# Performance work log

Measured on AMD Instinct MI355X. Metric: run time of the kernel, lower is better.

## Reference

```python
import jax, jax.numpy as jnp
import numpy as np
import math

B, T, XD, H, DD, P = 512, 256, 128, 512, 16, 32
IN = 2 * XD + DD  # GRUCell input size


def _init(key, shape, fan):
    stdv = 1.0 / math.sqrt(fan)
    return jax.random.uniform(key, shape, jnp.float32, -stdv, stdv)


def setup_inputs() -> dict:
    key = jax.random.key(0)
    ks = jax.random.split(key, 32)
    inp = {
        "values": jax.random.normal(ks[0], (B, T, XD), jnp.float32),
        "lens": jnp.full((B,), T, dtype=jnp.int32),  # lens[0] == max_len
        "static": jax.random.normal(ks[1], (B, DD), jnp.float32),
        "times": jax.random.uniform(ks[2], (B, T, XD), jnp.float32),
        "masks": (jax.random.uniform(ks[3], (B, T, XD)) < 0.8).astype(jnp.float32),
        "prototype": jax.random.normal(ks[4], (P, H), jnp.float32),
        "proto": True,
        # temp_decay_h: Linear(x_dim -> hidden), custom uniform(-1/sqrt(H), 1/sqrt(H))
        "Wd": _init(ks[5], (H, XD), H), "bd": _init(ks[6], (H,), XD),
        # hist_reg: Linear(hidden -> x_dim)
        "Wh": _init(ks[7], (XD, H), H), "bh": _init(ks[8], (XD,), H),
        "Wf": _init(ks[9], (XD, XD), XD), "bf": _init(ks[10], (XD,), XD),
        # ProtoAttn Q/K/V: Linear(hidden -> hidden)
        "Wq": _init(ks[11], (H, H), H), "bq": _init(ks[12], (H,), H),
        "Wk": _init(ks[13], (H, H), H), "bk": _init(ks[14], (H,), H),
        "Wv": _init(ks[15], (H, H), H), "bv": _init(ks[16], (H,), H),
        # gating W: Linear(2*hidden -> 1)
        "Wg": _init(ks[17], (1, 2 * H), 2 * H), "bg": _init(ks[18], (1,), 2 * H),
        # GRUCell
        "Wih": _init(ks[19], (3 * H, IN), H), "Whh": _init(ks[20], (3 * H, H), H),
        "bih": _init(ks[21], (3 * H,), H), "bhh": _init(ks[22], (3 * H,), H),
    }
    return inp


def _forward(values, static, times, masks, prototype,
             Wd, bd, Wh, bh, Wf, bf, Wq, bq, Wk, bk, Wv, bv, Wg, bg,
             Wih, Whh, bih, bhh, lens, proto):
    feat_m = 1.0 - jnp.eye(XD, dtype=values.dtype)  # zero-diagonal mask
    gamma = jnp.exp(-jax.nn.relu(jnp.einsum("btx,hx->bth", times, Wd) + bd))
    # attention key/value do not depend on h -> precompute
    keyp = prototype @ Wk.T + bk      # [P,H]
    valp = prototype @ Wv.T + bv      # [P,H]
    scale = 1.0 / math.sqrt(P)
    valid = (jnp.arange(T)[:, None] < lens[None, :]).astype(values.dtype)  # [T,B]

    xs = (jnp.swapaxes(values, 0, 1),  # [T,B,XD]
          jnp.swapaxes(masks, 0, 1),   # [T,B,XD]
          jnp.swapaxes(gamma, 0, 1),   # [T,B,H]
          valid[:, :, None])           # [T,B,1]

    h0 = jnp.zeros((B, H), values.dtype)
    xh0 = jnp.zeros((B, XD), values.dtype)

    def step(carry, xt):
        h, x_h = carry
        x, m, g, v = xt
        if proto:
            q = h @ Wq.T + bq                          # [B,H]
            score = (q @ keyp.T) * scale               # [B,P]
            attn = jax.nn.softmax(score, axis=-1)      # dropout omitted (eval)
            h1 = attn @ valp                           # [B,H]
            alpha = jax.nn.sigmoid(jnp.concatenate([h, h1], axis=1) @ Wg.T + bg)
            h = alpha * h + (1.0 - alpha) * h1
        h = h * g
        x_h = jnp.where(v > 0, h @ Wh.T + bh, x_h)
        x_c = m * x + (1.0 - m) * x_h
        z_h = x_c @ (Wf * feat_m).T + bf
        z_c = m * x + (1.0 - m) * z_h
        inp = jnp.concatenate([z_c, m, static], axis=1)
        gx = inp @ Wih.T + bih
        gh = h @ Whh.T + bhh
        xr, xz, xn = jnp.split(gx, 3, axis=1)
        hr, hz, hn = jnp.split(gh, 3, axis=1)
        r = jax.nn.sigmoid(xr + hr)
        z = jax.nn.sigmoid(xz + hz)
        n = jnp.tanh(xn + r * hn)
        h_new = (1.0 - z) * n + z * h
        h = jnp.where(v > 0, h_new, h)
        return (h, x_h), (h, x_c, z_c)

    (hN, _), (hs, x_cs, z_cs) = jax.lax.scan(step, (h0, xh0), xs)
    hs = jnp.swapaxes(hs, 0, 1)
    x_cs = jnp.swapaxes(x_cs, 0, 1)
    z_cs = jnp.swapaxes(z_cs, 0, 1)
    return hs, hN, x_cs, z_cs


def reference(values, lens, static, times, masks, prototype, proto,
              Wd, bd, Wh, bh, Wf, bf, Wq, bq, Wk, bk, Wv, bv, Wg, bg,
              Wih, Whh, bih, bhh):
    return _forward(values, static, times, masks, prototype,
                    Wd, bd, Wh, bh, Wf, bf, Wq, bq, Wk, bk, Wv, bv, Wg, bg,
                    Wih, Whh, bih, bhh, lens, bool(proto))
```

## Files before the change

kernel.cpp:

```cpp
#include <hip/hip_runtime.h>

#define NB 256
#define NT 512

#define Bv 512
#define Tv 256
#define XDv 128
#define Hv 512
#define DDv 16
#define Pv 32

typedef short s8 __attribute__((ext_vector_type(8)));
typedef float f4 __attribute__((ext_vector_type(4)));

#define OFF_KEYP 2048
#define OFF_VALP (OFF_KEYP + 16384)
#define OFF_MF   (OFF_VALP + 16384)
#define OFF_C    (OFF_MF + 16384)
#define OFF_VWG  (OFF_C + 32)
#define OFF_FRG  (OFF_VWG + 32)
#define US_WD   0
#define US_MS   65536
#define US_VP   81920
#define US_WH   98304
#define US_WF   163840
#define US_WHH  180224
#define US_WIH  966656
#define US_END  1409024
#define OFF_H   (OFF_FRG + (US_END/2))

#define OUT_HS  0
#define OUT_HN  (Bv*Tv*Hv)
#define OUT_XCS (OUT_HN + Bv*Hv)
#define OUT_ZCS (OUT_XCS + Bv*Tv*XDv)

struct Smem {
  unsigned short hA[32*520];
  unsigned short tA[32*136];
  unsigned short xcA[32*136];
  unsigned short inpA[32*296];
  unsigned short aA[32*40];
  unsigned short mA[32*136];
  unsigned short xhS[32*128];
  float xvS[32*132];
  float scS[32*34];
  float ghS[3*32*33];
  float gxS[3*32*33];
  float hp32[32*32];
  float al[32], rsm[32], cS[32], vwgS[32];
};

__device__ __forceinline__ unsigned short f2b(float f) {
  union { float f; unsigned int u; } x{f};
  unsigned int r = x.u + 0x7fffu + ((x.u >> 16) & 1u);
  return (unsigned short)(r >> 16);
}
__device__ __forceinline__ float b2f(unsigned short u) {
  union { unsigned int u; float f; } x{(unsigned int)u << 16};
  return x.f;
}
__device__ __forceinline__ float sig_f(float x) { return 1.f / (1.f + __expf(-x)); }
__device__ __forceinline__ float tanh_f(float x) {
  x = fminf(fmaxf(x, -15.f), 15.f);
  float e = __expf(2.f * x);
  return (e - 1.f) / (e + 1.f);
}
__device__ __forceinline__ s8 pack8(const float* p) {
  f4 a = *(const f4*)p; f4 b = *(const f4*)(p + 4);
  s8 r;
  r[0]=(short)f2b(a[0]); r[1]=(short)f2b(a[1]); r[2]=(short)f2b(a[2]); r[3]=(short)f2b(a[3]);
  r[4]=(short)f2b(b[0]); r[5]=(short)f2b(b[1]); r[6]=(short)f2b(b[2]); r[7]=(short)f2b(b[3]);
  return r;
}

__device__ __forceinline__ void gridbar(unsigned int* bar, unsigned int& lgen, int bid) {
  __syncthreads();
  if (threadIdx.x == 0) {
    __threadfence();
    const unsigned int target = ++lgen;
    unsigned int* grp = bar + (bid >> 4)*16;
    const unsigned int a =
        __hip_atomic_fetch_add(grp, 1u, __ATOMIC_ACQ_REL, __HIP_MEMORY_SCOPE_AGENT);
    if (a == 15u) {
      __hip_atomic_store(grp, 0u, __ATOMIC_RELAXED, __HIP_MEMORY_SCOPE_AGENT);
      const unsigned int r =
          __hip_atomic_fetch_add(bar + 384, 1u, __ATOMIC_ACQ_REL, __HIP_MEMORY_SCOPE_AGENT);
      if (r == 15u) {
        __hip_atomic_store(bar + 384, 0u, __ATOMIC_RELAXED, __HIP_MEMORY_SCOPE_AGENT);
        __hip_atomic_store(bar + 400, target, __ATOMIC_RELEASE, __HIP_MEMORY_SCOPE_AGENT);
      }
    }
    while (__hip_atomic_load(bar + 400, __ATOMIC_RELAXED, __HIP_MEMORY_SCOPE_AGENT) < target)
      __builtin_amdgcn_s_sleep(2);
    __threadfence();
  }
  __syncthreads();
}

__device__ __forceinline__ void rgbar_nf(unsigned int* bar, unsigned int& lgen, int rg) {
  __syncthreads();
  if (threadIdx.x == 0) {
    const unsigned int target = ++lgen;
    unsigned int* cnt = bar + 512 + rg*64;
    unsigned int* flg = cnt + 32;
    const unsigned int a =
        __hip_atomic_fetch_add(cnt, 1u, __ATOMIC_RELAXED, __HIP_MEMORY_SCOPE_AGENT);
    if (a == 15u) {
      __hip_atomic_store(cnt, 0u, __ATOMIC_RELAXED, __HIP_MEMORY_SCOPE_AGENT);
      asm volatile("s_waitcnt vmcnt(0)" ::: "memory");
      __hip_atomic_store(flg, target, __ATOMIC_RELAXED, __HIP_MEMORY_SCOPE_AGENT);
    } else {
      while (__hip_atomic_load(flg, __ATOMIC_RELAXED, __HIP_MEMORY_SCOPE_AGENT) < target)
        __builtin_amdgcn_s_sleep(2);
    }
  }
  __syncthreads();
}

#define SWZ(DST, NTILES, KT_, EXPR)                                            \
  { const int tot = (NTILES)*(KT_)*512;                                        \
    for (int f = gtid; f < tot; f += NB*NT) {                                  \
      const int e = f & 7, lane_ = (f >> 3) & 63, rem = f >> 9;                \
      const int kt = rem % (KT_), nt = rem / (KT_);                            \
      const int n = nt*16 + (lane_ & 15);                                      \
      const int k = kt*32 + ((lane_ >> 4) & 3)*8 + e;                          \
      (DST)[f] = f2b((EXPR));                                                  \
    } }

#define MFMA(a,b,c) __builtin_amdgcn_mfma_f32_16x16x32_bf16((a),(b),(c),0,0,0)
#define FRAG(P,idx) (*(const s8*)&(P)[((size_t)(idx))*8])

__global__ __launch_bounds__(NT, 2)
void rits_main(const float* __restrict__ values, const int* __restrict__ lens,
               const float* __restrict__ statc, const float* __restrict__ times,
               const float* __restrict__ masks, const float* __restrict__ prototype,
               const int* __restrict__ protoflag,
               const float* __restrict__ Wd, const float* __restrict__ bd,
               const float* __restrict__ Wh, const float* __restrict__ bh,
               const float* __restrict__ Wf, const float* __restrict__ bf,
               const float* __restrict__ Wq, const float* __restrict__ bq,
               const float* __restrict__ Wk, const float* __restrict__ bk,
               const float* __restrict__ Wv, const float* __restrict__ bv,
               const float* __restrict__ Wg, const float* __restrict__ bg,
               const float* __restrict__ Wih, const float* __restrict__ Whh,
               const float* __restrict__ bih, const float* __restrict__ bhh,
               float* __restrict__ out, float* __restrict__ ws)
{
  const int bid = blockIdx.x, tid = threadIdx.x;
  const int gtid = bid*NT + tid;
  const int wv = tid >> 6, ln = tid & 63;
  const int l15 = ln & 15, l4 = ln >> 4;
  const int cg = (bid & 7)*2 + ((bid >> 7) & 1);
  const int rg = (bid >> 3) & 15;
  const int r0 = rg*32, c0 = cg*32;
  unsigned int* bar = (unsigned int*)ws;
  unsigned int lgenG = 0, lgenR = 0;
  unsigned short* frg = (unsigned short*)(ws + OFF_FRG);
  const unsigned short* wdW  = frg + US_WD;
  const unsigned short* msW  = frg + US_MS;
  const unsigned short* vpW  = frg + US_VP;
  const unsigned short* whW  = frg + US_WH;
  const unsigned short* wfW  = frg + US_WF;
  const unsigned short* whhW = frg + US_WHH;
  const unsigned short* wihW = frg + US_WIH;
  unsigned int* wsH = (unsigned int*)(ws + OFF_H);

  __shared__ Smem L;
  const bool proto = protoflag[0] != 0;
  const float scale = 0.17677669529663687f;

  for (int o = gtid; o < 2*Pv*Hv; o += NB*NT) {
    const int which = o >> 14, rem = o & 16383;
    const int p = rem >> 9, j = rem & 511;
    const float* W = which ? Wv : Wk;
    const float* bb = which ? bv : bk;
    const float* pr = prototype + p*Hv;
    const float* wr = W + j*Hv;
    float s = bb[j];
    #pragma unroll 4
    for (int k = 0; k < Hv; ++k) s += pr[k]*wr[k];
    ws[(which ? OFF_VALP : OFF_KEYP) + p*Hv + j] = s;
  }
  SWZ(frg + US_WD, 32, 4,  Wd[n*XDv + k])
  SWZ(frg + US_WH, 8, 16,  Wh[n*Hv + k])
  SWZ(frg + US_WF, 8, 4,   (n == k ? 0.f : Wf[n*XDv + k]))
  SWZ(frg + US_WHH, 96, 16,
      Whh[((size_t)(n >> 9)*Hv + (((n >> 5) & 15)*32 + ((n >> 4) & 1)*16 + (n & 15)))*Hv + k])
  SWZ(frg + US_WIH, 96, 9,
      (k < 272 ? Wih[((size_t)(n >> 9)*Hv + (((n >> 5) & 15)*32 + ((n >> 4) & 1)*16 + (n & 15)))*272 + k] : 0.f))
  gridbar(bar, lgenG, bid);

  {
    const float* keyp = ws + OFF_KEYP;
    const float* valp = ws + OFF_VALP;
    for (int o = gtid; o < Pv*Hv; o += NB*NT) {
      const int p = o >> 9, kc = o & 511;
      float s = 0.f;
      #pragma unroll 4
      for (int j = 0; j < Hv; ++j) s += keyp[p*Hv + j]*Wq[j*Hv + kc];
      ws[OFF_MF + o] = s;
    }
    if (gtid < 32) {
      float s = 0.f;
      for (int j = 0; j < Hv; ++j) s += bq[j]*keyp[gtid*Hv + j];
      ws[OFF_C + gtid] = s;
    } else if (gtid < 64) {
      const int p = gtid - 32;
      float s = 0.f;
      for (int j = 0; j < Hv; ++j) s += valp[p*Hv + j]*Wg[Hv + j];
      ws[OFF_VWG + p] = s;
    }
  }
  gridbar(bar, lgenG, bid);

  SWZ(frg + US_MS, 2, 16, (ws + OFF_MF)[n*Hv + k])
  SWZ(frg + US_VP, 32, 1, (ws + OFF_VALP)[k*Hv + n])
  gridbar(bar, lgenG, bid);

  for (int o = tid; o < 32*128; o += NT) L.xhS[o] = 0;
  if (tid < 32) { L.cS[tid] = ws[OFF_C + tid]; L.vwgS[tid] = ws[OFF_VWG + tid]; }
  for (int o = tid; o < 32*40; o += NT) {
    const int row = o / 40, cc = o % 40;
    L.inpA[row*296 + 256 + cc] =
        (cc < DDv) ? f2b(statc[(r0 + row)*DDv + cc]) : (unsigned short)0;
  }

  const int xcol = wv*16 + l15;
  const float bhR = bh[xcol], bfR = bf[xcol];
  int lensA[8];
  #pragma unroll
  for (int rt = 0; rt < 2; ++rt)
    #pragma unroll
    for (int i = 0; i < 4; ++i)
      lensA[rt*4 + i] = lens[r0 + rt*16 + l4*4 + i];
  float wgr[8];
  if (wv >= 4) {
    #pragma unroll
    for (int e = 0; e < 8; ++e) wgr[e] = Wg[ln*8 + e];
  }
  f4 bdW;
  #pragma unroll
  for (int q = 0; q < 4; ++q) bdW[q] = bd[wv*64 + q*16 + l15];
  const int crow = tid >> 5, cjj = tid & 31;
  float bihR[3], bhhR[3];
  #pragma unroll
  for (int g = 0; g < 3; ++g) { bihR[g] = bih[g*Hv + c0 + cjj]; bhhR[g] = bhh[g*Hv + c0 + cjj]; }
  const int lensG0 = lens[r0 + crow], lensG1 = lens[r0 + crow + 16];
  const float bg0 = bg[0];

  float pv[8], pm[8], pt[8];
  #pragma unroll
  for (int i = 0; i < 8; ++i) {
    const int o = i*NT + tid, row = o >> 7, col = o & 127;
    const size_t a = ((size_t)(r0 + row)*Tv + 0)*XDv + col;
    pv[i] = values[a]; pm[i] = masks[a]; pt[i] = times[a];
  }
  __syncthreads();

  for (int t = 0; t < Tv; ++t) {
    #pragma unroll
    for (int i = 0; i < 8; ++i) {
      const int o = i*NT + tid, row = o >> 7, col = o & 127;
      L.xvS[row*132 + col] = pv[i];
      L.mA[row*136 + col]  = f2b(pm[i]);
      L.tA[row*136 + col]  = f2b(pt[i]);
    }
    {
      const int tn = (t + 1 < Tv) ? t + 1 : t;
      #pragma unroll
      for (int i = 0; i < 8; ++i) {
        const int o = i*NT + tid, row = o >> 7, col = o & 127;
        const size_t a = ((size_t)(r0 + row)*Tv + tn)*XDv + col;
        pv[i] = values[a]; pm[i] = masks[a]; pt[i] = times[a];
      }
    }
    if (t > 0) {
      const unsigned int* src = wsH + ((t - 1) & 1)*131072;
      #pragma unroll
      for (int i = 0; i < 16; ++i) {
        const int o = i*NT + tid, row = o >> 8, cp = o & 255;
        const unsigned int v = __hip_atomic_load(
            &src[(size_t)(r0 + row)*256 + cp], __ATOMIC_RELAXED, __HIP_MEMORY_SCOPE_AGENT);
        ((unsigned int*)&L.hA[row*520])[cp] = v;
      }
    } else {
      for (int o = tid; o < 32*256; o += NT) {
        const int row = o >> 8, cp = o & 255;
        ((unsigned int*)&L.hA[row*520])[cp] = 0u;
      }
    }
    __syncthreads();

    if (proto) {
      if (wv < 4) {
        const int rt = wv >> 1, nt = wv & 1;
        f4 acc = {0.f,0.f,0.f,0.f};
        #pragma unroll
        for (int kt = 0; kt < 16; ++kt) {
          s8 a = *(const s8*)&L.hA[(rt*16 + l15)*520 + kt*32 + l4*8];
          acc = MFMA(a, FRAG(msW, (nt*16 + kt)*64 + ln), acc);
        }
        #pragma unroll
        for (int i = 0; i < 4; ++i)
          L.scS[(rt*16 + l4*4 + i)*34 + nt*16 + l15] = acc[i];
      } else {
        #pragma unroll
        for (int rr = 0; rr < 8; ++rr) {
          const int row = (wv - 4)*8 + rr;
          s8 hv8 = *(const s8*)&L.hA[row*520 + ln*8];
          float s = 0.f;
          #pragma unroll
          for (int e = 0; e < 8; ++e) s += b2f((unsigned short)hv8[e]) * wgr[e];
          s += __shfl_xor(s, 1);  s += __shfl_xor(s, 2);  s += __shfl_xor(s, 4);
          s += __shfl_xor(s, 8);  s += __shfl_xor(s, 16); s += __shfl_xor(s, 32);
          if (ln == 0) L.scS[row*34 + 32] = s;
        }
      }
    }
    __syncthreads();

    if (proto && wv == 0 && ln < 32) {
      const int r = ln;
      float mx = -1e30f;
      #pragma unroll 8
      for (int p = 0; p < 32; ++p)
        mx = fmaxf(mx, (L.scS[r*34 + p] + L.cS[p]) * scale);
      float sm = 0.f, a1 = 0.f;
      #pragma unroll 8
      for (int p = 0; p < 32; ++p) {
        float e = __expf((L.scS[r*34 + p] + L.cS[p]) * scale - mx);
        sm += e; a1 += e * L.vwgS[p];
        L.aA[r*40 + p] = f2b(e);
      }
      const float rs = 1.f / sm;
      L.rsm[r] = rs;
      L.al[r] = sig_f(L.scS[r*34 + 32] + a1*rs + bg0);
    }
    __syncthreads();

    #pragma unroll
    for (int q = 0; q < 4; ++q) {
      const int nt = wv*4 + q;
      const int col = nt*16 + l15;
      #pragma unroll
      for (int rt = 0; rt < 2; ++rt) {
        f4 g = {0.f,0.f,0.f,0.f};
        #pragma unroll
        for (int kt = 0; kt < 4; ++kt) {
          s8 a = *(const s8*)&L.tA[(rt*16 + l15)*136 + kt*32 + l4*8];
          g = MFMA(a, FRAG(wdW, (nt*4 + kt)*64 + ln), g);
        }
        f4 h1 = {0.f,0.f,0.f,0.f};
        if (proto) {
          s8 a = *(const s8*)&L.aA[(rt*16 + l15)*40 + l4*8];
          h1 = MFMA(a, FRAG(vpW, nt*64 + ln), h1);
        }
        #pragma unroll
        for (int i = 0; i < 4; ++i) {
          const int row = rt*16 + l4*4 + i;
          const float gam = __expf(-fmaxf(g[i] + bdW[q], 0.f));
          const float hbf = b2f(L.hA[row*520 + col]);
          float hp;
          if (proto) {
            const float av = L.al[row];
            hp = (av*hbf + (1.f - av)*h1[i]*L.rsm[row]) * gam;
          } else hp = hbf * gam;
          L.hA[row*520 + col] = f2b(hp);
          const unsigned cc = (unsigned)(col - c0);
          if (cc < 32u) L.hp32[row*32 + cc] = hp;
        }
      }
    }
    __syncthreads();

    #pragma unroll
    for (int rt = 0; rt < 2; ++rt) {
      f4 acc = {0.f,0.f,0.f,0.f};
      #pragma unroll
      for (int kt = 0; kt < 16; ++kt) {
        s8 a = *(const s8*)&L.hA[(rt*16 + l15)*520 + kt*32 + l4*8];
        acc = MFMA(a, FRAG(whW, (wv*16 + kt)*64 + ln), acc);
      }
      #pragma unroll
      for (int i = 0; i < 4; ++i) {
        const int row = rt*16 + l4*4 + i;
        const int b = r0 + row;
        float xh = acc[i] + bhR;
        if (t < lensA[rt*4 + i]) L.xhS[row*128 + xcol] = f2b(xh);
        else                     xh = b2f(L.xhS[row*128 + xcol]);
        const float xv = L.xvS[row*132 + xcol], mv = b2f(L.mA[row*136 + xcol]);
        const float xc = mv*xv + (1.f - mv)*xh;
        if (cg == 0) out[OUT_XCS + ((size_t)b*Tv + t)*XDv + xcol] = xc;
        L.xcA[row*136 + xcol] = f2b(xc);
      }
    }
    __syncthreads();

    #pragma unroll
    for (int rt = 0; rt < 2; ++rt) {
      f4 acc = {0.f,0.f,0.f,0.f};
      #pragma unroll
      for (int kt = 0; kt < 4; ++kt) {
        s8 a = *(const s8*)&L.xcA[(rt*16 + l15)*136 + kt*32 + l4*8];
        acc = MFMA(a, FRAG(wfW, (wv*4 + kt)*64 + ln), acc);
      }
      #pragma unroll
      for (int i = 0; i < 4; ++i) {
        const int row = rt*16 + l4*4 + i;
        const float xv = L.xvS[row*132 + xcol], mv = b2f(L.mA[row*136 + xcol]);
        const float zc = mv*xv + (1.f - mv)*(acc[i] + bfR);
        if (cg == 0) out[OUT_ZCS + ((size_t)(r0 + row)*Tv + t)*XDv + xcol] = zc;
        L.inpA[row*296 + xcol]       = f2b(zc);
        L.inpA[row*296 + 128 + xcol] = f2b(mv);
      }
    }
    __syncthreads();

    if (wv < 6) {
      const int g = wv >> 1, cLoc = (wv & 1)*16 + l15;
      const int ntG = g*32 + cg*2 + (wv & 1);
      #pragma unroll
      for (int rt = 0; rt < 2; ++rt) {
        f4 acc = {0.f,0.f,0.f,0.f};
        #pragma unroll
        for (int kt = 0; kt < 16; ++kt) {
          s8 a = *(const s8*)&L.hA[(rt*16 + l15)*520 + kt*32 + l4*8];
          acc = MFMA(a, FRAG(whhW, (ntG*16 + kt)*64 + ln), acc);
        }
        #pragma unroll
        for (int i = 0; i < 4; ++i)
          L.ghS[g*1056 + (rt*16 + l4*4 + i)*33 + cLoc] = acc[i];
      }
    } else {
      #pragma unroll
      for (int cti = 0; cti < 3; ++cti) {
        const int ct = (wv - 6)*3 + cti;
        const int g = ct >> 1, cLoc = (ct & 1)*16 + l15;
        const int ntG = g*32 + cg*2 + (ct & 1);
        #pragma unroll
        for (int rt = 0; rt < 2; ++rt) {
          f4 acc = {0.f,0.f,0.f,0.f};
          #pragma unroll
          for (int kt = 0; kt < 9; ++kt) {
            s8 a = *(const s8*)&L.inpA[(rt*16 + l15)*296 + kt*32 + l4*8];
            acc = MFMA(a, FRAG(wihW, (ntG*9 + kt)*64 + ln), acc);
          }
          #pragma unroll
          for (int i = 0; i < 4; ++i)
            L.gxS[g*1056 + (rt*16 + l4*4 + i)*33 + cLoc] = acc[i];
        }
      }
    }
    __syncthreads();

    unsigned int* dst = wsH + (t & 1)*131072;
    #pragma unroll
    for (int cc = 0; cc < 2; ++cc) {
      const int row = crow + cc*16;
      const int b = r0 + row, jc = c0 + cjj;
      const float xr = L.gxS[row*33 + cjj]        + bihR[0];
      const float xz = L.gxS[1056 + row*33 + cjj] + bihR[1];
      const float xn = L.gxS[2112 + row*33 + cjj] + bihR[2];
      const float hr = L.ghS[row*33 + cjj]        + bhhR[0];
      const float hz = L.ghS[1056 + row*33 + cjj] + bhhR[1];
      const float hn = L.ghS[2112 + row*33 + cjj] + bhhR[2];
      const float r = sig_f(xr + hr), z = sig_f(xz + hz);
      const float n = tanh_f(xn + r*hn);
      const float hpv = L.hp32[row*32 + cjj];
      const int lb = cc ? lensG1 : lensG0;
      const float hfv = (t < lb) ? ((1.f - z)*n + z*hpv) : hpv;
      out[OUT_HS + ((size_t)b*Tv + t)*Hv + jc] = hfv;
      if (t == Tv - 1) out[OUT_HN + (size_t)b*Hv + jc] = hfv;
      const float partner = __shfl_xor(hfv, 1);
      if ((cjj & 1) == 0) {
        const unsigned int pk = (unsigned int)f2b(hfv) | ((unsigned int)f2b(partner) << 16);
        __hip_atomic_store(&dst[(size_t)b*256 + cg*16 + (cjj >> 1)], pk,
                           __ATOMIC_RELAXED, __HIP_MEMORY_SCOPE_AGENT);
      }
    }
    rgbar_nf(bar, lgenR, rg);
  }
}

extern "C" void kernel_launch(void* const* d_in, const int* in_sizes, int n_in,
                              void* d_out, int out_size, void* d_ws, size_t ws_size,
                              hipStream_t stream) {
  (void)in_sizes; (void)n_in; (void)out_size; (void)ws_size;
  hipMemsetAsync(d_ws, 0, 8192, stream);
  rits_main<<<NB, NT, 0, stream>>>(
      (const float*)d_in[0],  (const int*)d_in[1],   (const float*)d_in[2],
      (const float*)d_in[3],  (const float*)d_in[4], (const float*)d_in[5],
      (const int*)d_in[6],
      (const float*)d_in[7],  (const float*)d_in[8],
      (const float*)d_in[9],  (const float*)d_in[10],
      (const float*)d_in[11], (const float*)d_in[12],
      (const float*)d_in[13], (const float*)d_in[14],
      (const float*)d_in[15], (const float*)d_in[16],
      (const float*)d_in[17], (const float*)d_in[18],
      (const float*)d_in[19], (const float*)d_in[20],
      (const float*)d_in[21], (const float*)d_in[22],
      (const float*)d_in[23], (const float*)d_in[24],
      (float*)d_out, (float*)d_ws);
}
```

Baseline: 17.00 ms.

## Merge Whh GEMM into hist-reg stage, add nontemporal IO, swap block-to-tile mapping

The recurrent h@Whh GEMM now shares A-fragment loads with the h@Wh hist-regression GEMM inside one stage. The Wih GEMM is redistributed across waves 0-5, and some MFMA operand loads are hoisted into registers. The h-state load from global memory moves ahead of the input staging, input loads and output stores become nontemporal, and the row-group/column-group mapping of block IDs is swapped. The intent is to cut per-step work imbalance and the serial chain of stages, and to keep streaming traffic out of cache, at the cost of more register pressure and a different L2 locality pattern.

```diff
diff --git a/kernel.cpp b/kernel.cpp
--- a/kernel.cpp
+++ b/kernel.cpp
@@ -129,6 +129,7 @@
 
 #define MFMA(a,b,c) __builtin_amdgcn_mfma_f32_16x16x32_bf16((a),(b),(c),0,0,0)
 #define FRAG(P,idx) (*(const s8*)&(P)[((size_t)(idx))*8])
+#define NTST(v,p) __builtin_nontemporal_store((v),(p))
 
 __global__ __launch_bounds__(NT, 2)
 void rits_main(const float* __restrict__ values, const int* __restrict__ lens,
@@ -150,8 +151,8 @@
   const int gtid = bid*NT + tid;
   const int wv = tid >> 6, ln = tid & 63;
   const int l15 = ln & 15, l4 = ln >> 4;
-  const int cg = (bid & 7)*2 + ((bid >> 7) & 1);
-  const int rg = (bid >> 3) & 15;
+  const int rg = (bid & 7)*2 + ((bid >> 7) & 1);
+  const int cg = (bid >> 3) & 15;
   const int r0 = rg*32, c0 = cg*32;
   unsigned int* bar = (unsigned int*)ws;
   unsigned int lgenG = 0, lgenR = 0;
@@ -253,11 +254,28 @@
   for (int i = 0; i < 8; ++i) {
     const int o = i*NT + tid, row = o >> 7, col = o & 127;
     const size_t a = ((size_t)(r0 + row)*Tv + 0)*XDv + col;
-    pv[i] = values[a]; pm[i] = masks[a]; pt[i] = times[a];
+    pv[i] = __builtin_nontemporal_load(&values[a]);
+    pm[i] = __builtin_nontemporal_load(&masks[a]);
+    pt[i] = __builtin_nontemporal_load(&times[a]);
   }
   __syncthreads();
 
   for (int t = 0; t < Tv; ++t) {
+    if (t > 0) {
+      const unsigned int* src = wsH + ((t - 1) & 1)*131072;
+      #pragma unroll
+      for (int i = 0; i < 16; ++i) {
+        const int o = i*NT + tid, row = o >> 8, cp = o & 255;
+        const unsigned int v = __hip_atomic_load(
+            &src[(size_t)(r0 + row)*256 + cp], __ATOMIC_RELAXED, __HIP_MEMORY_SCOPE_AGENT);
+        ((unsigned int*)&L.hA[row*520])[cp] = v;
+      }
+    } else {
+      for (int o = tid; o < 32*256; o += NT) {
+        const int row = o >> 8, cp = o & 255;
+        ((unsigned int*)&L.hA[row*520])[cp] = 0u;
+      }
+    }
     #pragma unroll
     for (int i = 0; i < 8; ++i) {
       const int o = i*NT + tid, row = o >> 7, col = o & 127;
@@ -271,22 +289,9 @@
       for (int i = 0; i < 8; ++i) {
         const int o = i*NT + tid, row = o >> 7, col = o & 127;
         const size_t a = ((size_t)(r0 + row)*Tv + tn)*XDv + col;
-        pv[i] = values[a]; pm[i] = masks[a]; pt[i] = times[a];
-      }
-    }
-    if (t > 0) {
-      const unsigned int* src = wsH + ((t - 1) & 1)*131072;
-      #pragma unroll
-      for (int i = 0; i < 16; ++i) {
-        const int o = i*NT + tid, row = o >> 8, cp = o & 255;
-        const unsigned int v = __hip_atomic_load(
-            &src[(size_t)(r0 + row)*256 + cp], __ATOMIC_RELAXED, __HIP_MEMORY_SCOPE_AGENT);
-        ((unsigned int*)&L.hA[row*520])[cp] = v;
-      }
-    } else {
-      for (int o = tid; o < 32*256; o += NT) {
-        const int row = o >> 8, cp = o & 255;
-        ((unsigned int*)&L.hA[row*520])[cp] = 0u;
+        pv[i] = __builtin_nontemporal_load(&values[a]);
+        pm[i] = __builtin_nontemporal_load(&masks[a]);
+        pt[i] = __builtin_nontemporal_load(&times[a]);
       }
     }
     __syncthreads();
@@ -338,117 +343,122 @@
     }
     __syncthreads();
 
-    #pragma unroll
-    for (int q = 0; q < 4; ++q) {
-      const int nt = wv*4 + q;
-      const int col = nt*16 + l15;
+    {
+      s8 ta[2][4]; s8 aa[2];
       #pragma unroll
       for (int rt = 0; rt < 2; ++rt) {
-        f4 g = {0.f,0.f,0.f,0.f};
-        #pragma unroll
-        for (int kt = 0; kt < 4; ++kt) {
-          s8 a = *(const s8*)&L.tA[(rt*16 + l15)*136 + kt*32 + l4*8];
-          g = MFMA(a, FRAG(wdW, (nt*4 + kt)*64 + ln), g);
-        }
-        f4 h1 = {0.f,0.f,0.f,0.f};
-        if (proto) {
-          s8 a = *(const s8*)&L.aA[(rt*16 + l15)*40 + l4*8];
-          h1 = MFMA(a, FRAG(vpW, nt*64 + ln), h1);
+        #pragma unroll
+        for (int kt = 0; kt < 4; ++kt)
+          ta[rt][kt] = *(const s8*)&L.tA[(rt*16 + l15)*136 + kt*32 + l4*8];
+        if (proto) aa[rt] = *(const s8*)&L.aA[(rt*16 + l15)*40 + l4*8];
+      }
+      #pragma unroll
+      for (int q = 0; q < 4; ++q) {
+        const int nt = wv*4 + q;
+        const int col = nt*16 + l15;
+        #pragma unroll
+        for (int rt = 0; rt < 2; ++rt) {
+          f4 g = {0.f,0.f,0.f,0.f};
+          #pragma unroll
+          for (int kt = 0; kt < 4; ++kt)
+            g = MFMA(ta[rt][kt], FRAG(wdW, (nt*4 + kt)*64 + ln), g);
+          f4 h1 = {0.f,0.f,0.f,0.f};
+          if (proto) h1 = MFMA(aa[rt], FRAG(vpW, nt*64 + ln), h1);
+          #pragma unroll
+          for (int i = 0; i < 4; ++i) {
+            const int row = rt*16 + l4*4 + i;
+            const float gam = __expf(-fmaxf(g[i] + bdW[q], 0.f));
+            const float hbf = b2f(L.hA[row*520 + col]);
+            float hp;
+            if (proto) {
+              const float av = L.al[row];
+              hp = (av*hbf + (1.f - av)*h1[i]*L.rsm[row]) * gam;
+            } else hp = hbf * gam;
+            L.hA[row*520 + col] = f2b(hp);
+            const unsigned cc = (unsigned)(col - c0);
+            if (cc < 32u) L.hp32[row*32 + cc] = hp;
+          }
+        }
+      }
+    }
+    __syncthreads();
+
+    {
+      const int g = wv >> 1, hf = wv & 1;
+      const int ntG = g*32 + cg*2 + hf;
+      #pragma unroll
+      for (int rt = 0; rt < 2; ++rt) {
+        f4 accX = {0.f,0.f,0.f,0.f};
+        f4 accG = {0.f,0.f,0.f,0.f};
+        #pragma unroll
+        for (int kt = 0; kt < 16; ++kt) {
+          s8 a = *(const s8*)&L.hA[(rt*16 + l15)*520 + kt*32 + l4*8];
+          accX = MFMA(a, FRAG(whW, (wv*16 + kt)*64 + ln), accX);
+          if (wv < 6) accG = MFMA(a, FRAG(whhW, (ntG*16 + kt)*64 + ln), accG);
         }
         #pragma unroll
         for (int i = 0; i < 4; ++i) {
           const int row = rt*16 + l4*4 + i;
-          const float gam = __expf(-fmaxf(g[i] + bdW[q], 0.f));
-          const float hbf = b2f(L.hA[row*520 + col]);
-          float hp;
-          if (proto) {
-            const float av = L.al[row];
-            hp = (av*hbf + (1.f - av)*h1[i]*L.rsm[row]) * gam;
-          } else hp = hbf * gam;
-          L.hA[row*520 + col] = f2b(hp);
-          const unsigned cc = (unsigned)(col - c0);
-          if (cc < 32u) L.hp32[row*32 + cc] = hp;
-        }
-      }
-    }
-    __syncthreads();
-
-    #pragma unroll
-    for (int rt = 0; rt < 2; ++rt) {
-      f4 acc = {0.f,0.f,0.f,0.f};
-      #pragma unroll
-      for (int kt = 0; kt < 16; ++kt) {
-        s8 a = *(const s8*)&L.hA[(rt*16 + l15)*520 + kt*32 + l4*8];
-        acc = MFMA(a, FRAG(whW, (wv*16 + kt)*64 + ln), acc);
-      }
-      #pragma unroll
-      for (int i = 0; i < 4; ++i) {
-        const int row = rt*16 + l4*4 + i;
-        const int b = r0 + row;
-        float xh = acc[i] + bhR;
-        if (t < lensA[rt*4 + i]) L.xhS[row*128 + xcol] = f2b(xh);
-        else                     xh = b2f(L.xhS[row*128 + xcol]);
-        const float xv = L.xvS[row*132 + xcol], mv = b2f(L.mA[row*136 + xcol]);
-        const float xc = mv*xv + (1.f - mv)*xh;
-        if (cg == 0) out[OUT_XCS + ((size_t)b*Tv + t)*XDv + xcol] = xc;
-        L.xcA[row*136 + xcol] = f2b(xc);
-      }
-    }
-    __syncthreads();
-
-    #pragma unroll
-    for (int rt = 0; rt < 2; ++rt) {
-      f4 acc = {0.f,0.f,0.f,0.f};
-      #pragma unroll
-      for (int kt = 0; kt < 4; ++kt) {
-        s8 a = *(const s8*)&L.xcA[(rt*16 + l15)*136 + kt*32 + l4*8];
-        acc = MFMA(a, FRAG(wfW, (wv*4 + kt)*64 + ln), acc);
-      }
-      #pragma unroll
-      for (int i = 0; i < 4; ++i) {
-        const int row = rt*16 + l4*4 + i;
-        const float xv = L.xvS[row*132 + xcol], mv = b2f(L.mA[row*136 + xcol]);
-        const float zc = mv*xv + (1.f - mv)*(acc[i] + bfR);
-        if (cg == 0) out[OUT_ZCS + ((size_t)(r0 + row)*Tv + t)*XDv + xcol] = zc;
-        L.inpA[row*296 + xcol]       = f2b(zc);
-        L.inpA[row*296 + 128 + xcol] = f2b(mv);
-      }
-    }
-    __syncthreads();
-
-    if (wv < 6) {
-      const int g = wv >> 1, cLoc = (wv & 1)*16 + l15;
-      const int ntG = g*32 + cg*2 + (wv & 1);
-      #pragma unroll
-      for (int rt = 0; rt < 2; ++rt) {
-        f4 acc = {0.f,0.f,0.f,0.f};
-        #pragma unroll
-        for (int kt = 0; kt < 16; ++kt) {
-          s8 a = *(const s8*)&L.hA[(rt*16 + l15)*520 + kt*32 + l4*8];
-          acc = MFMA(a, FRAG(whhW, (ntG*16 + kt)*64 + ln), acc);
-        }
-        #pragma unroll
-        for (int i = 0; i < 4; ++i)
-          L.ghS[g*1056 + (rt*16 + l4*4 + i)*33 + cLoc] = acc[i];
-      }
-    } else {
-      #pragma unroll
-      for (int cti = 0; cti < 3; ++cti) {
-        const int ct = (wv - 6)*3 + cti;
-        const int g = ct >> 1, cLoc = (ct & 1)*16 + l15;
-        const int ntG = g*32 + cg*2 + (ct & 1);
-        #pragma unroll
-        for (int rt = 0; rt < 2; ++rt) {
-          f4 acc = {0.f,0.f,0.f,0.f};
-          #pragma unroll
-          for (int kt = 0; kt < 9; ++kt) {
-            s8 a = *(const s8*)&L.inpA[(rt*16 + l15)*296 + kt*32 + l4*8];
-            acc = MFMA(a, FRAG(wihW, (ntG*9 + kt)*64 + ln), acc);
-          }
+          const int b = r0 + row;
+          float xh = accX[i] + bhR;
+          if (t < lensA[rt*4 + i]) L.xhS[row*128 + xcol] = f2b(xh);
+          else                     xh = b2f(L.xhS[row*128 + xcol]);
+          const float xv = L.xvS[row*132 + xcol], mv = b2f(L.mA[row*136 + xcol]);
+          const float xc = mv*xv + (1.f - mv)*xh;
+          if (cg == 0) NTST(xc, &out[OUT_XCS + ((size_t)b*Tv + t)*XDv + xcol]);
+          L.xcA[row*136 + xcol] = f2b(xc);
+        }
+        if (wv < 6) {
+          const int cLoc = hf*16 + l15;
           #pragma unroll
           for (int i = 0; i < 4; ++i)
-            L.gxS[g*1056 + (rt*16 + l4*4 + i)*33 + cLoc] = acc[i];
-        }
+            L.ghS[g*1056 + (rt*16 + l4*4 + i)*33 + cLoc] = accG[i];
+        }
+      }
+    }
+    __syncthreads();
+
+    {
+      #pragma unroll
+      for (int rt = 0; rt < 2; ++rt) {
+        s8 af[4];
+        #pragma unroll
+        for (int kt = 0; kt < 4; ++kt)
+          af[kt] = *(const s8*)&L.xcA[(rt*16 + l15)*136 + kt*32 + l4*8];
+        f4 acc = {0.f,0.f,0.f,0.f};
+        #pragma unroll
+        for (int kt = 0; kt < 4; ++kt)
+          acc = MFMA(af[kt], FRAG(wfW, (wv*4 + kt)*64 + ln), acc);
+        #pragma unroll
+        for (int i = 0; i < 4; ++i) {
+          const int row = rt*16 + l4*4 + i;
+          const float xv = L.xvS[row*132 + xcol], mv = b2f(L.mA[row*136 + xcol]);
+          const float zc = mv*xv + (1.f - mv)*(acc[i] + bfR);
+          if (cg == 0) NTST(zc, &out[OUT_ZCS + ((size_t)(r0 + row)*Tv + t)*XDv + xcol]);
+          L.inpA[row*296 + xcol]       = f2b(zc);
+          L.inpA[row*296 + 128 + xcol] = f2b(mv);
+        }
+      }
+    }
+    __syncthreads();
+
+    if (wv < 6) {
+      const int g = wv >> 1, hf = wv & 1;
+      const int ntG = g*32 + cg*2 + hf;
+      const int cLoc = hf*16 + l15;
+      #pragma unroll
+      for (int rt = 0; rt < 2; ++rt) {
+        s8 af[9];
+        #pragma unroll
+        for (int kt = 0; kt < 9; ++kt)
+          af[kt] = *(const s8*)&L.inpA[(rt*16 + l15)*296 + kt*32 + l4*8];
+        f4 acc = {0.f,0.f,0.f,0.f};
+        #pragma unroll
+        for (int kt = 0; kt < 9; ++kt)
+          acc = MFMA(af[kt], FRAG(wihW, (ntG*9 + kt)*64 + ln), acc);
+        #pragma unroll
+        for (int i = 0; i < 4; ++i)
+          L.gxS[g*1056 + (rt*16 + l4*4 + i)*33 + cLoc] = acc[i];
       }
     }
     __syncthreads();
@@ -469,8 +479,8 @@
       const float hpv = L.hp32[row*32 + cjj];
       const int lb = cc ? lensG1 : lensG0;
       const float hfv = (t < lb) ? ((1.f - z)*n + z*hpv) : hpv;
-      out[OUT_HS + ((size_t)b*Tv + t)*Hv + jc] = hfv;
-      if (t == Tv - 1) out[OUT_HN + (size_t)b*Hv + jc] = hfv;
+      NTST(hfv, &out[OUT_HS + ((size_t)b*Tv + t)*Hv + jc]);
+      if (t == Tv - 1) NTST(hfv, &out[OUT_HN + (size_t)b*Hv + jc]);
       const float partner = __shfl_xor(hfv, 1);
       if ((cjj & 1) == 0) {
         const unsigned int pk = (unsigned int)f2b(hfv) | ((unsigned int)f2b(partner) << 16);
```

Measured after the change: 18.95 ms. +11.5%, slower.
